# Performance work log

Measured on AMD Instinct MI355X. Metric: run time of the kernel, lower is better.

Reference implementation:

```python
import jax, jax.numpy as jnp
import numpy as np

N_HEADS = 16


def _apply_rope(x, cos, sin):
    # x: [B, H, S, hd]; cos/sin: [>=S, hd/2]
    S = x.shape[2]
    cos = cos[None, None, :S]
    sin = sin[None, None, :S]
    x1, x2 = x[..., ::2], x[..., 1::2]
    # interleaved rotate, matching torch stack(...).flatten(-2)
    return jnp.stack([x1 * cos - x2 * sin, x1 * sin + x2 * cos], axis=-1).reshape(x.shape)


def setup_inputs() -> dict:
    key = jax.random.key(0)
    B, S, D = 2, 2048, 1024
    hd = D // N_HEADS
    k1, k2, k3 = jax.random.split(key, 3)
    x = jax.random.normal(k1, (B, S, D), dtype=jnp.float32)
    # standard RoPE tables (theta=10000)
    inv_freq = 1.0 / (10000.0 ** (np.arange(0, hd, 2, dtype=np.float32) / hd))  # [hd/2]
    freqs = np.outer(np.arange(S, dtype=np.float32), inv_freq)  # [S, hd/2]
    rope_cos = jnp.asarray(np.cos(freqs), dtype=jnp.float32)
    rope_sin = jnp.asarray(np.sin(freqs), dtype=jnp.float32)
    W_qkv = jax.random.normal(k2, (D, 3 * D), dtype=jnp.float32) * (D ** -0.5)
    W_out = jax.random.normal(k3, (D, D), dtype=jnp.float32) * (D ** -0.5)
    return {"x": x, "rope_cos": rope_cos, "rope_sin": rope_sin, "W_qkv": W_qkv, "W_out": W_out}


def reference(x, rope_cos, rope_sin, W_qkv, W_out):
    B, S, D = x.shape
    H = N_HEADS
    hd = D // H
    qkv = (x @ W_qkv).reshape(B, S, 3, H, hd)  # fused QKV projection
    q = qkv[:, :, 0].transpose(0, 2, 1, 3)  # [B,H,S,hd]
    k = qkv[:, :, 1].transpose(0, 2, 1, 3)
    v = qkv[:, :, 2].transpose(0, 2, 1, 3)
    q = _apply_rope(q, rope_cos, rope_sin)
    k = _apply_rope(k, rope_cos, rope_sin)
    scale = hd ** -0.5
    scores = jnp.einsum('bhqd,bhkd->bhqk', q, k) * scale  # [B,H,S,S]
    causal = jnp.tril(jnp.ones((S, S), dtype=bool))
    scores = jnp.where(causal, scores, jnp.finfo(scores.dtype).min)
    attn = jax.nn.softmax(scores, axis=-1)
    out = jnp.einsum('bhqk,bhkd->bhqd', attn, v)  # [B,H,S,hd]
    out = out.transpose(0, 2, 1, 3).reshape(B, S, D)
    return out @ W_out  # dropout is identity in eval mode
```

## Files before the change

### kernel.cpp

```cpp
#include <hip/hip_runtime.h>
#include <hip/hip_bf16.h>
#include <stdint.h>

typedef short bf16x8 __attribute__((ext_vector_type(8)));
typedef short bf16x4 __attribute__((ext_vector_type(4)));
typedef float f32x4 __attribute__((ext_vector_type(4)));

#define HD 64
#define NH 16
#define SEQ 2048
#define BATCH 2
#define DM 1024
#define TOK (BATCH * SEQ)

__device__ __forceinline__ unsigned short f2bf(float f) {
    union { float f; unsigned u; } a; a.f = f;
    unsigned r = a.u + 0x7fffu + ((a.u >> 16) & 1u);
    return (unsigned short)(r >> 16);
}
__device__ __forceinline__ float bf2f(unsigned short u) {
    union { unsigned u; float f; } a; a.u = ((unsigned)u) << 16;
    return a.f;
}

__device__ __forceinline__ unsigned pkbf16(float a, float b) {
    union { __hip_bfloat162 h; unsigned u; } cv;
    cv.h = __float22bfloat162_rn(make_float2(a, b));
    return cv.u;
}

__device__ __forceinline__ float fexp2(float x) {
#if __has_builtin(__builtin_amdgcn_exp2f)
    return __builtin_amdgcn_exp2f(x);
#else
    return exp2f(x);
#endif
}
__device__ __forceinline__ float frcp(float x) {
#if __has_builtin(__builtin_amdgcn_rcpf)
    return __builtin_amdgcn_rcpf(x);
#else
    return 1.0f / x;
#endif
}

__device__ __forceinline__ f32x4 mfma16(bf16x4 a, bf16x4 b, f32x4 c) {
#if defined(__HIP_DEVICE_COMPILE__)
    return __builtin_amdgcn_mfma_f32_16x16x16bf16_1k(a, b, c, 0, 0, 0);
#else
    (void)a; (void)b;
    return c;
#endif
}

__device__ __forceinline__ void gld_lds16(const unsigned short* g, unsigned short* l) {
#if __has_builtin(__builtin_amdgcn_global_load_lds)
    __builtin_amdgcn_global_load_lds(
        (const __attribute__((address_space(1))) unsigned int*)g,
        (__attribute__((address_space(3))) unsigned int*)l, 16, 0, 0);
#else
    *(bf16x8*)l = *(const bf16x8*)g;
#endif
}

__global__ void __launch_bounds__(256) k_prep(const float* __restrict__ x,
                                              unsigned short* __restrict__ xb,
                                              const float* __restrict__ wqkv,
                                              unsigned short* __restrict__ wqkvt,
                                              const float* __restrict__ wout,
                                              unsigned short* __restrict__ woutt) {
    int bid = blockIdx.x;
    int tid = threadIdx.x;
    if (bid < 4096) {
        int i = (bid * 256 + tid) * 4;
        float4 v = *(const float4*)(x + i);
        union { ushort4 v; unsigned short s[4]; } o;
        o.s[0] = f2bf(v.x); o.s[1] = f2bf(v.y); o.s[2] = f2bf(v.z); o.s[3] = f2bf(v.w);
        *(ushort4*)(xb + i) = o.v;
        return;
    }
    const float* W; unsigned short* Wt; int N, t;
    if (bid < 7168) { W = wqkv; Wt = wqkvt; N = 3 * DM; t = bid - 4096; }
    else            { W = wout; Wt = woutt; N = DM;     t = bid - 7168; }
    int ntx = N >> 5;
    int bx = t % ntx, by = t / ntx;
    int tx = tid & 31, ty = tid >> 5;
    __shared__ float tile[32][33];
    for (int r = 0; r < 4; ++r) {
        int k = by * 32 + ty + r * 8;
        int n = bx * 32 + tx;
        tile[ty + r * 8][tx] = W[(size_t)k * N + n];
    }
    __syncthreads();
    for (int r = 0; r < 4; ++r) {
        int n = bx * 32 + ty + r * 8;
        int k = by * 32 + tx;
        Wt[(size_t)n * DM + k] = f2bf(tile[tx][ty + r * 8]);
    }
}

#define BKK 32

__global__ void __launch_bounds__(128) k_gemm_qkv(const unsigned short* __restrict__ A,
                                                  const unsigned short* __restrict__ Bt,
                                                  unsigned short* __restrict__ qbuf,
                                                  unsigned short* __restrict__ kbuf,
                                                  unsigned short* __restrict__ vt) {
    constexpr int K = DM;
    __shared__ unsigned short As0[128 * BKK];
    __shared__ unsigned short As1[128 * BKK];
    __shared__ unsigned short Bs0[64 * BKK];
    __shared__ unsigned short Bs1[64 * BKK];
    int tid = threadIdx.x;
    int lane = tid & 63, wave = tid >> 6;
    int lin = (int)blockIdx.x + (int)blockIdx.y * 48;
    int nl = (lin & 7) * 192 + (lin >> 3);
    int bx = nl % 48, by = nl / 48;
    int row0 = by * 128, col0 = bx * 64;
    int wm = wave * 64;
    int fr = lane & 15, quad = lane >> 4;

    f32x4 zero4 = {0.f, 0.f, 0.f, 0.f};
    f32x4 acc[4][4];
    for (int i = 0; i < 4; ++i)
        for (int j = 0; j < 4; ++j) acc[i][j] = zero4;

    auto stage = [&](unsigned short* Ad, unsigned short* Bd, int k0) {
        for (int i = 0; i < 4; ++i) {
            int idx = i * 128 + tid;
            int r = idx >> 2, kc = idx & 3;
            int kk = (kc ^ (r & 3)) * 8;
            gld_lds16(A + (size_t)(row0 + r) * K + k0 + kk, Ad + (i * 128 + wave * 64) * 8);
        }
        for (int i = 0; i < 2; ++i) {
            int idx = i * 128 + tid;
            int r = idx >> 2, kc = idx & 3;
            int kk = (kc ^ (r & 3)) * 8;
            gld_lds16(Bt + (size_t)(col0 + r) * K + k0 + kk, Bd + (i * 128 + wave * 64) * 8);
        }
    };
    auto compute = [&](const unsigned short* Al, const unsigned short* Bl) {
        bf16x8 af[4], bfr[4];
        for (int i = 0; i < 4; ++i) {
            int rr = wm + i * 16 + fr;
            af[i] = *(const bf16x8*)&Al[rr * BKK + ((quad ^ (rr & 3)) * 8)];
        }
        for (int j = 0; j < 4; ++j) {
            int rr = j * 16 + fr;
            bfr[j] = *(const bf16x8*)&Bl[rr * BKK + ((quad ^ (rr & 3)) * 8)];
        }
        for (int i = 0; i < 4; ++i)
            for (int j = 0; j < 4; ++j)
                acc[i][j] = __builtin_amdgcn_mfma_f32_16x16x32_bf16(af[i], bfr[j], acc[i][j], 0, 0, 0);
    };

    stage(As0, Bs0, 0);
    __syncthreads();
    for (int k0 = 0; k0 < K; k0 += 2 * BKK) {
        if (k0 + BKK < K) stage(As1, Bs1, k0 + BKK);
        compute(As0, Bs0);
        __syncthreads();
        if (k0 + 2 * BKK < K) stage(As0, Bs0, k0 + 2 * BKK);
        compute(As1, Bs1);
        __syncthreads();
    }

    int rq = quad * 4;
    int cq = fr;
    for (int i = 0; i < 4; ++i)
        for (int j = 0; j < 4; ++j)
            for (int reg = 0; reg < 4; ++reg) {
                int row = row0 + wm + i * 16 + rq + reg;
                int col = col0 + j * 16 + cq;
                float v = acc[i][j][reg];
                int which = col >> 10;
                int hc = col & 1023;
                int h = hc >> 6, d = hc & 63;
                int b = row >> 11, s = row & (SEQ - 1);
                int bh = b * NH + h;
                unsigned short bv = f2bf(v);
                if (which == 0)      qbuf[((size_t)bh * SEQ + s) * HD + d] = bv;
                else if (which == 1) kbuf[((size_t)bh * SEQ + s) * HD + d] = bv;
                else                 vt[((size_t)bh * HD + d) * SEQ + s] = bv;
            }
}

__global__ void __launch_bounds__(128) k_gemm_out(const unsigned short* __restrict__ A,
                                                  const unsigned short* __restrict__ Bt,
                                                  float* __restrict__ C) {
    constexpr int K = DM;
    __shared__ unsigned short As0[128 * BKK];
    __shared__ unsigned short As1[128 * BKK];
    __shared__ unsigned short Bs0[64 * BKK];
    __shared__ unsigned short Bs1[64 * BKK];
    int tid = threadIdx.x;
    int lane = tid & 63, wave = tid >> 6;
    int lin = (int)blockIdx.x + (int)blockIdx.y * 16;
    int nl = (lin & 7) * 64 + (lin >> 3);
    int bx = nl & 15, by = nl >> 4;
    int row0 = by * 128, col0 = bx * 64;
    int wm = wave * 64;
    int fr = lane & 15, quad = lane >> 4;

    f32x4 zero4 = {0.f, 0.f, 0.f, 0.f};
    f32x4 acc[4][4];
    for (int i = 0; i < 4; ++i)
        for (int j = 0; j < 4; ++j) acc[i][j] = zero4;

    auto stage = [&](unsigned short* Ad, unsigned short* Bd, int k0) {
        for (int i = 0; i < 4; ++i) {
            int idx = i * 128 + tid;
            int r = idx >> 2, kc = idx & 3;
            int kk = (kc ^ (r & 3)) * 8;
            gld_lds16(A + (size_t)(row0 + r) * K + k0 + kk, Ad + (i * 128 + wave * 64) * 8);
        }
        for (int i = 0; i < 2; ++i) {
            int idx = i * 128 + tid;
            int r = idx >> 2, kc = idx & 3;
            int kk = (kc ^ (r & 3)) * 8;
            gld_lds16(Bt + (size_t)(col0 + r) * K + k0 + kk, Bd + (i * 128 + wave * 64) * 8);
        }
    };
    auto compute = [&](const unsigned short* Al, const unsigned short* Bl) {
        bf16x8 af[4], bfr[4];
        for (int i = 0; i < 4; ++i) {
            int rr = wm + i * 16 + fr;
            af[i] = *(const bf16x8*)&Al[rr * BKK + ((quad ^ (rr & 3)) * 8)];
        }
        for (int j = 0; j < 4; ++j) {
            int rr = j * 16 + fr;
            bfr[j] = *(const bf16x8*)&Bl[rr * BKK + ((quad ^ (rr & 3)) * 8)];
        }
        for (int i = 0; i < 4; ++i)
            for (int j = 0; j < 4; ++j)
                acc[i][j] = __builtin_amdgcn_mfma_f32_16x16x32_bf16(af[i], bfr[j], acc[i][j], 0, 0, 0);
    };

    stage(As0, Bs0, 0);
    __syncthreads();
    for (int k0 = 0; k0 < K; k0 += 2 * BKK) {
        if (k0 + BKK < K) stage(As1, Bs1, k0 + BKK);
        compute(As0, Bs0);
        __syncthreads();
        if (k0 + 2 * BKK < K) stage(As0, Bs0, k0 + 2 * BKK);
        compute(As1, Bs1);
        __syncthreads();
    }

    int rq = quad * 4;
    int cq = fr;
    for (int i = 0; i < 4; ++i)
        for (int j = 0; j < 4; ++j)
            for (int reg = 0; reg < 4; ++reg) {
                int row = row0 + wm + i * 16 + rq + reg;
                int col = col0 + j * 16 + cq;
                C[(size_t)row * DM + col] = acc[i][j][reg];
            }
}

__global__ void k_rope(unsigned short* __restrict__ qbuf, unsigned short* __restrict__ kbuf,
                       const float* __restrict__ cosb, const float* __restrict__ sinb) {
    int t = blockIdx.x * 256 + threadIdx.x;
    int c = t & 7;
    int row = (t >> 3) & 65535;
    int which = t >> 19;
    unsigned short* p = (which ? kbuf : qbuf) + (size_t)row * HD + c * 8;
    float sc = which ? 1.0f : (0.125f * 1.44269504f);
    int s = row & (SEQ - 1);
    const float* cs = cosb + s * 32 + c * 4;
    const float* sn = sinb + s * 32 + c * 4;
    bf16x8 v = *(const bf16x8*)p;
    bf16x8 o;
    for (int i = 0; i < 4; ++i) {
        float x1 = bf2f((unsigned short)v[2 * i]);
        float x2 = bf2f((unsigned short)v[2 * i + 1]);
        float cc = cs[i], ss = sn[i];
        o[2 * i]     = (short)f2bf((x1 * cc - x2 * ss) * sc);
        o[2 * i + 1] = (short)f2bf((x1 * ss + x2 * cc) * sc);
    }
    *(bf16x8*)p = o;
}

__global__ void __launch_bounds__(128, 2) k_attn(const unsigned short* __restrict__ qbuf,
                                                 const unsigned short* __restrict__ kbuf,
                                                 const unsigned short* __restrict__ vt,
                                                 unsigned short* __restrict__ obuf) {
    __shared__ unsigned short Ks0[64 * 64];
    __shared__ unsigned short Ks1[64 * 64];
    __shared__ unsigned short Vs0[64 * 64];
    __shared__ unsigned short Vs1[64 * 64];

    int tid = threadIdx.x;
    int lane = tid & 63, wave = tid >> 6;
    int bh = blockIdx.y;
    int b = bh >> 4, h = bh & 15;
    int p = ((int)blockIdx.x + (int)blockIdx.y) & 31;
    int fr = lane & 15, quad = lane >> 4, sw = fr & 7;
    int Qb0 = (2 * p + wave) * 16;
    int Qb1 = (127 - 2 * p - wave) * 16;
    int KT = ((127 - 2 * p) >> 2) + 1;

    const unsigned short* Qb = qbuf + (size_t)bh * SEQ * HD;
    const unsigned short* Kb = kbuf + (size_t)bh * SEQ * HD;
    const unsigned short* Vb = vt + (size_t)bh * HD * SEQ;

    bf16x8 qf[2][2];
    for (int s = 0; s < 2; ++s) {
        int qrow = (s ? Qb1 : Qb0) + fr;
        qf[s][0] = *(const bf16x8*)(Qb + (size_t)qrow * HD + quad * 8);
        qf[s][1] = *(const bf16x8*)(Qb + (size_t)qrow * HD + 32 + quad * 8);
    }

    f32x4 zero4 = {0.f, 0.f, 0.f, 0.f};
    f32x4 o[2][4];
    for (int s = 0; s < 2; ++s)
        for (int j = 0; j < 4; ++j) o[s][j] = zero4;
    float l[2] = {0.f, 0.f};

    auto stage = [&](int kb, unsigned short* Kd, unsigned short* Vd) {
        for (int a = 0; a < 4; ++a) {
            int idx = a * 128 + tid;
            int r = idx >> 3;
            int lg = (idx & 7) ^ (r & 7);
            gld_lds16(Kb + (size_t)(kb + r) * HD + lg * 8, Kd + (a * 128 + wave * 64) * 8);
            gld_lds16(Vb + (size_t)r * SEQ + kb + lg * 8, Vd + (a * 128 + wave * 64) * 8);
        }
    };

    auto compute = [&](int kt, const unsigned short* Kd, const unsigned short* Vd) {
        int kb = kt * 64;
        bf16x8 ka[4], kc[4];
        for (int g = 0; g < 4; ++g) {
            int r = g * 16 + fr;
            ka[g] = *(const bf16x8*)&Kd[r * 64 + ((quad ^ sw) * 8)];
            kc[g] = *(const bf16x8*)&Kd[r * 64 + (((quad + 4) ^ sw) * 8)];
        }
        bf16x4 vf[4][4];
        for (int g = 0; g < 4; ++g)
            for (int db = 0; db < 4; ++db) {
                int d = db * 16 + fr;
                int pg = ((2 * g + (quad >> 1)) ^ sw) * 8 + (quad & 1) * 4;
                vf[g][db] = *(const bf16x4*)&Vd[d * 64 + pg];
            }
        for (int s = 0; s < 2; ++s) {
            int Qs = s ? Qb1 : Qb0;
            if (kb > Qs + 15) continue;
            f32x4 sg[4];
            for (int g = 0; g < 4; ++g) {
                f32x4 z = zero4;
                z = __builtin_amdgcn_mfma_f32_16x16x32_bf16(ka[g], qf[s][0], z, 0, 0, 0);
                z = __builtin_amdgcn_mfma_f32_16x16x32_bf16(kc[g], qf[s][1], z, 0, 0, 0);
                sg[g] = z;
            }
            if (kb + 63 > Qs) {
                int q = Qs + fr;
                for (int g = 0; g < 4; ++g)
                    for (int reg = 0; reg < 4; ++reg)
                        if (kb + g * 16 + quad * 4 + reg > q) sg[g][reg] = -1e30f;
            }
            bf16x4 pf[4];
            for (int g = 0; g < 4; ++g) {
                float p0 = fexp2(sg[g][0]);
                float p1 = fexp2(sg[g][1]);
                float p2 = fexp2(sg[g][2]);
                float p3 = fexp2(sg[g][3]);
                l[s] += (p0 + p1) + (p2 + p3);
                union { bf16x4 v; unsigned u[2]; } pc;
                pc.u[0] = pkbf16(p0, p1);
                pc.u[1] = pkbf16(p2, p3);
                pf[g] = pc.v;
            }
            for (int g = 0; g < 4; ++g)
                for (int db = 0; db < 4; ++db)
                    o[s][db] = mfma16(pf[g], vf[g][db], o[s][db]);
        }
    };

    stage(0, Ks0, Vs0);
    __syncthreads();
    for (int kt = 0; kt < KT; kt += 2) {
        if (kt + 1 < KT) stage((kt + 1) * 64, Ks1, Vs1);
        compute(kt, Ks0, Vs0);
        __syncthreads();
        if (kt + 1 < KT) {
            if (kt + 2 < KT) stage((kt + 2) * 64, Ks0, Vs0);
            compute(kt + 1, Ks1, Vs1);
            __syncthreads();
        }
    }

    for (int s = 0; s < 2; ++s) {
        float ll = l[s];
        ll += __shfl_xor(ll, 16);
        ll += __shfl_xor(ll, 32);
        float linv[4];
        for (int reg = 0; reg < 4; ++reg)
            linv[reg] = frcp(__shfl(ll, quad * 4 + reg));
        int Qs = s ? Qb1 : Qb0;
        for (int db = 0; db < 4; ++db)
            for (int reg = 0; reg < 4; ++reg) {
                int row = Qs + quad * 4 + reg;
                int d = db * 16 + fr;
                obuf[((size_t)(b * SEQ + row)) * DM + h * HD + d] = f2bf(o[s][db][reg] * linv[reg]);
            }
    }
}

extern "C" void kernel_launch(void* const* d_in, const int* in_sizes, int n_in,
                              void* d_out, int out_size, void* d_ws, size_t ws_size,
                              hipStream_t stream) {
    const float* x    = (const float*)d_in[0];
    const float* rc   = (const float*)d_in[1];
    const float* rs   = (const float*)d_in[2];
    const float* wqkv = (const float*)d_in[3];
    const float* wout = (const float*)d_in[4];
    float* out = (float*)d_out;

    char* ws = (char*)d_ws;
    size_t off = 0;
    auto alloc = [&](size_t bytes) {
        char* p = ws + off;
        off += (bytes + 255) & ~(size_t)255;
        return p;
    };
    unsigned short* xb    = (unsigned short*)alloc((size_t)TOK * DM * 2);
    unsigned short* wqkvt = (unsigned short*)alloc((size_t)3 * DM * DM * 2);
    unsigned short* woutt = (unsigned short*)alloc((size_t)DM * DM * 2);
    unsigned short* qbuf  = (unsigned short*)alloc((size_t)BATCH * NH * SEQ * HD * 2);
    unsigned short* kbuf  = (unsigned short*)alloc((size_t)BATCH * NH * SEQ * HD * 2);
    unsigned short* vtb   = (unsigned short*)alloc((size_t)BATCH * NH * SEQ * HD * 2);
    unsigned short* obuf  = (unsigned short*)alloc((size_t)TOK * DM * 2);

    k_prep<<<8192, 256, 0, stream>>>(x, xb, wqkv, wqkvt, wout, woutt);
    k_gemm_qkv<<<dim3(3 * DM / 64, TOK / 128), 128, 0, stream>>>(xb, wqkvt, qbuf, kbuf, vtb);
    k_rope<<<4096, 256, 0, stream>>>(qbuf, kbuf, rc, rs);
    k_attn<<<dim3(SEQ / 64, BATCH * NH), 128, 0, stream>>>(qbuf, kbuf, vtb, obuf);
    k_gemm_out<<<dim3(DM / 64, TOK / 128), 128, 0, stream>>>(obuf, woutt, out);
}
```

Baseline: 198.2 us.

## Restructure QKV GEMM into 256x256 tiles with phased prefetch pipeline

Rewrites the QKV projection GEMM to use 512-thread blocks computing 256x256 output tiles with a K step of 64. The global-to-LDS prefetch of the next tile is split into four quarters, interleaved with MFMA phases under explicit waitcnt, barriers, sched_barrier and setprio. The aim is more data reuse per block and overlap of loads with matrix math. The cost is only 192 blocks, which may underfill the GPU, plus heavy register pressure and 128KB of LDS.

```diff
diff --git a/kernel.cpp b/kernel.cpp
--- a/kernel.cpp
+++ b/kernel.cpp
@@ -41,6 +41,12 @@
     return __builtin_amdgcn_rcpf(x);
 #else
     return 1.0f / x;
+#endif
+}
+
+__device__ __forceinline__ void schedbar() {
+#if defined(__HIP_DEVICE_COMPILE__)
+    __builtin_amdgcn_sched_barrier(0);
 #endif
 }
 
@@ -101,84 +107,121 @@
 
 #define BKK 32
 
-__global__ void __launch_bounds__(128) k_gemm_qkv(const unsigned short* __restrict__ A,
-                                                  const unsigned short* __restrict__ Bt,
-                                                  unsigned short* __restrict__ qbuf,
-                                                  unsigned short* __restrict__ kbuf,
-                                                  unsigned short* __restrict__ vt) {
+#define QBM 256
+#define QBK 64
+
+__global__ void __launch_bounds__(512, 1) k_gemm_qkv(const unsigned short* __restrict__ A,
+                                                     const unsigned short* __restrict__ Bt,
+                                                     unsigned short* __restrict__ qbuf,
+                                                     unsigned short* __restrict__ kbuf,
+                                                     unsigned short* __restrict__ vt) {
     constexpr int K = DM;
-    __shared__ unsigned short As0[128 * BKK];
-    __shared__ unsigned short As1[128 * BKK];
-    __shared__ unsigned short Bs0[64 * BKK];
-    __shared__ unsigned short Bs1[64 * BKK];
+    constexpr int NT = K / QBK;
+    __shared__ __attribute__((aligned(16))) unsigned short As[2][QBM * QBK];
+    __shared__ __attribute__((aligned(16))) unsigned short Bs[2][QBM * QBK];
+
     int tid = threadIdx.x;
     int lane = tid & 63, wave = tid >> 6;
-    int lin = (int)blockIdx.x + (int)blockIdx.y * 48;
-    int nl = (lin & 7) * 192 + (lin >> 3);
-    int bx = nl % 48, by = nl / 48;
-    int row0 = by * 128, col0 = bx * 64;
-    int wm = wave * 64;
+    int wm = wave >> 2, wn = wave & 3;
     int fr = lane & 15, quad = lane >> 4;
 
+    int lin = (int)blockIdx.x;
+    int nl = (lin & 7) * 24 + (lin >> 3);
+    int bx = nl % 12, by = nl / 12;
+    int row0 = by * 256, col0 = bx * 256;
+
     f32x4 zero4 = {0.f, 0.f, 0.f, 0.f};
-    f32x4 acc[4][4];
-    for (int i = 0; i < 4; ++i)
+    f32x4 acc[8][4];
+#pragma unroll
+    for (int i = 0; i < 8; ++i)
+#pragma unroll
         for (int j = 0; j < 4; ++j) acc[i][j] = zero4;
 
-    auto stage = [&](unsigned short* Ad, unsigned short* Bd, int k0) {
-        for (int i = 0; i < 4; ++i) {
-            int idx = i * 128 + tid;
-            int r = idx >> 2, kc = idx & 3;
-            int kk = (kc ^ (r & 3)) * 8;
-            gld_lds16(A + (size_t)(row0 + r) * K + k0 + kk, Ad + (i * 128 + wave * 64) * 8);
-        }
+    auto stageHalf = [&](int kt, int half) {
+        int buf = kt & 1;
+        const unsigned short* G;
+        unsigned short* D;
+        if (half < 2) { G = Bt + (size_t)(col0 + half * 128) * K; D = &Bs[buf][half * 128 * QBK]; }
+        else          { G = A  + (size_t)(row0 + (half - 2) * 128) * K; D = &As[buf][(half - 2) * 128 * QBK]; }
+#pragma unroll
         for (int i = 0; i < 2; ++i) {
-            int idx = i * 128 + tid;
-            int r = idx >> 2, kc = idx & 3;
-            int kk = (kc ^ (r & 3)) * 8;
-            gld_lds16(Bt + (size_t)(col0 + r) * K + k0 + kk, Bd + (i * 128 + wave * 64) * 8);
-        }
-    };
-    auto compute = [&](const unsigned short* Al, const unsigned short* Bl) {
-        bf16x8 af[4], bfr[4];
-        for (int i = 0; i < 4; ++i) {
-            int rr = wm + i * 16 + fr;
-            af[i] = *(const bf16x8*)&Al[rr * BKK + ((quad ^ (rr & 3)) * 8)];
-        }
-        for (int j = 0; j < 4; ++j) {
-            int rr = j * 16 + fr;
-            bfr[j] = *(const bf16x8*)&Bl[rr * BKK + ((quad ^ (rr & 3)) * 8)];
-        }
-        for (int i = 0; i < 4; ++i)
-            for (int j = 0; j < 4; ++j)
-                acc[i][j] = __builtin_amdgcn_mfma_f32_16x16x32_bf16(af[i], bfr[j], acc[i][j], 0, 0, 0);
-    };
-
-    stage(As0, Bs0, 0);
-    __syncthreads();
-    for (int k0 = 0; k0 < K; k0 += 2 * BKK) {
-        if (k0 + BKK < K) stage(As1, Bs1, k0 + BKK);
-        compute(As0, Bs0);
-        __syncthreads();
-        if (k0 + 2 * BKK < K) stage(As0, Bs0, k0 + 2 * BKK);
-        compute(As1, Bs1);
-        __syncthreads();
-    }
-
-    int rq = quad * 4;
-    int cq = fr;
-    for (int i = 0; i < 4; ++i)
+            int s = i * 512 + tid;
+            int r = s >> 3, c = s & 7;
+            int g = c ^ (((r >> 1) & 3) << 1);
+            gld_lds16(G + (size_t)r * K + kt * QBK + g * 8, D + (i * 512 + wave * 64) * 8);
+        }
+    };
+    auto rdA = [&](int buf, int m, int kh) -> bf16x8 {
+        int rr = wm * 128 + m * 16 + fr;
+        int cc = (kh * 4 + quad) ^ (((rr >> 1) & 3) << 1);
+        return *(const bf16x8*)&As[buf][rr * QBK + cc * 8];
+    };
+    auto rdB = [&](int buf, int j, int kh) -> bf16x8 {
+        int rr = wn * 64 + j * 16 + fr;
+        int cc = (kh * 4 + quad) ^ (((rr >> 1) & 3) << 1);
+        return *(const bf16x8*)&Bs[buf][rr * QBK + cc * 8];
+    };
+
+    stageHalf(0, 0); stageHalf(0, 1); stageHalf(0, 2); stageHalf(0, 3);
+    asm volatile("s_waitcnt vmcnt(0)" ::: "memory");
+    __builtin_amdgcn_s_barrier();
+    schedbar();
+
+    for (int kt = 0; kt < NT; ++kt) {
+        int buf = kt & 1;
+        bool pre = (kt + 1 < NT);
+        bf16x8 bfr[4][2], af[2][2];
+#pragma unroll
+        for (int p = 0; p < 4; ++p) {
+            if (p == 0)      asm volatile("s_waitcnt vmcnt(1)" ::: "memory");
+            else if (p == 2) {
+                if (pre) asm volatile("s_waitcnt vmcnt(4)" ::: "memory");
+                else     asm volatile("s_waitcnt vmcnt(0)" ::: "memory");
+            }
+            __builtin_amdgcn_s_barrier();
+            schedbar();
+            if (p == 0) {
+#pragma unroll
+                for (int j = 0; j < 4; ++j) {
+                    bfr[j][0] = rdB(buf, j, 0);
+                    bfr[j][1] = rdB(buf, j, 1);
+                }
+            }
+#pragma unroll
+            for (int ii = 0; ii < 2; ++ii) {
+                af[ii][0] = rdA(buf, 2 * p + ii, 0);
+                af[ii][1] = rdA(buf, 2 * p + ii, 1);
+            }
+            if (pre) stageHalf(kt + 1, p);
+            asm volatile("s_waitcnt lgkmcnt(0)" ::: "memory");
+            schedbar();
+            __builtin_amdgcn_s_setprio(1);
+#pragma unroll
+            for (int ii = 0; ii < 2; ++ii)
+#pragma unroll
+                for (int j = 0; j < 4; ++j) {
+                    acc[2 * p + ii][j] = __builtin_amdgcn_mfma_f32_16x16x32_bf16(af[ii][0], bfr[j][0], acc[2 * p + ii][j], 0, 0, 0);
+                    acc[2 * p + ii][j] = __builtin_amdgcn_mfma_f32_16x16x32_bf16(af[ii][1], bfr[j][1], acc[2 * p + ii][j], 0, 0, 0);
+                }
+            __builtin_amdgcn_s_setprio(0);
+        }
+    }
+
+    int rq = quad * 4, cq = fr;
+#pragma unroll
+    for (int i = 0; i < 8; ++i)
+#pragma unroll
         for (int j = 0; j < 4; ++j)
+#pragma unroll
             for (int reg = 0; reg < 4; ++reg) {
-                int row = row0 + wm + i * 16 + rq + reg;
-                int col = col0 + j * 16 + cq;
-                float v = acc[i][j][reg];
+                int row = row0 + wm * 128 + i * 16 + rq + reg;
+                int col = col0 + wn * 64 + j * 16 + cq;
                 int which = col >> 10;
                 int hc = col & 1023;
                 int h = hc >> 6, d = hc & 63;
                 int b = row >> 11, s = row & (SEQ - 1);
                 int bh = b * NH + h;
-                unsigned short bv = f2bf(v);
+                unsigned short bv = f2bf(acc[i][j][reg]);
                 if (which == 0)      qbuf[((size_t)bh * SEQ + s) * HD + d] = bv;
                 else if (which == 1) kbuf[((size_t)bh * SEQ + s) * HD + d] = bv;
                 else                 vt[((size_t)bh * HD + d) * SEQ + s] = bv;
@@ -432,7 +475,7 @@
     unsigned short* obuf  = (unsigned short*)alloc((size_t)TOK * DM * 2);
 
     k_prep<<<8192, 256, 0, stream>>>(x, xb, wqkv, wqkvt, wout, woutt);
-    k_gemm_qkv<<<dim3(3 * DM / 64, TOK / 128), 128, 0, stream>>>(xb, wqkvt, qbuf, kbuf, vtb);
+    k_gemm_qkv<<<192, 512, 0, stream>>>(xb, wqkvt, qbuf, kbuf, vtb);
     k_rope<<<4096, 256, 0, stream>>>(qbuf, kbuf, rc, rs);
     k_attn<<<dim3(SEQ / 64, BATCH * NH), 128, 0, stream>>>(qbuf, kbuf, vtb, obuf);
     k_gemm_out<<<dim3(DM / 64, TOK / 128), 128, 0, stream>>>(obuf, woutt, out);
```

New measurement: 199.4 us. No clear change (+0.6%).
